# Kernel tuning notes

Measured on AMD Instinct MI355X. Metric: run time of the kernel, lower is better.

## Reference

```python
import jax, jax.numpy as jnp
import numpy as np

B, T = 512, 200
N_SKILLS, M, DK, DV, H = 1000, 50, 64, 64, 128


def setup_inputs() -> dict:
    key = jax.random.key(0)
    ks = jax.random.split(key, 12)
    inp = {
        'skill_seq': jax.random.randint(ks[0], (B, T), 0, N_SKILLS, dtype=jnp.int32),
        'correct_seq': jax.random.randint(ks[1], (B, T), 0, 2, dtype=jnp.int32),
        'mask': jnp.ones((B, T), dtype=jnp.float32),
        'skill_embed': jax.random.normal(ks[2], (N_SKILLS, DK), dtype=jnp.float32),
        'key_memory': jax.random.normal(ks[3], (M, DK), dtype=jnp.float32) * 0.1,
        'value_init': jnp.zeros((M, DV), dtype=jnp.float32),
        'interaction_embed': jax.random.normal(ks[4], (2 * N_SKILLS, DV), dtype=jnp.float32),
        'erase_W': jax.random.normal(ks[5], (DV, DV), dtype=jnp.float32) * 0.05,
        'erase_b': jnp.zeros((DV,), dtype=jnp.float32),
        'add_W': jax.random.normal(ks[6], (DV, DV), dtype=jnp.float32) * 0.05,
        'add_b': jnp.zeros((DV,), dtype=jnp.float32),
        'fc1_W': jax.random.normal(ks[7], (DK + DV, H), dtype=jnp.float32) * 0.05,
        'fc1_b': jnp.zeros((H,), dtype=jnp.float32),
        'fc2_W': jax.random.normal(ks[8], (H, 1), dtype=jnp.float32) * 0.05,
        'fc2_b': jnp.zeros((1,), dtype=jnp.float32),
    }
    return inp


def reference(skill_seq, correct_seq, mask, skill_embed, key_memory, value_init,
              interaction_embed, erase_W, erase_b, add_W, add_b,
              fc1_W, fc1_b, fc2_W, fc2_b):
    n_skills = skill_embed.shape[0]
    b = skill_seq.shape[0]
    # Time-invariant-per-step quantities are precomputed vectorized over (B,T):
    q = skill_embed[skill_seq]                                   # (B,T,dk)
    w = jax.nn.softmax(jnp.einsum('btk,mk->btm', q, key_memory), axis=-1)  # (B,T,M)
    v = interaction_embed[skill_seq + correct_seq * n_skills]    # (B,T,dv)
    e = jax.nn.sigmoid(v @ erase_W + erase_b)                    # (B,T,dv)
    a = jnp.tanh(v @ add_W + add_b)                              # (B,T,dv)

    def step(mem, inputs):
        # mem: (B,M,dv); read BEFORE write, matching the torch loop
        w_t, e_t, a_t = inputs                                   # (B,M),(B,dv),(B,dv)
        read = jnp.einsum('bm,bmv->bv', w_t, mem)                # (B,dv)
        we = w_t[:, :, None]                                     # (B,M,1)
        mem = mem * (1.0 - we * e_t[:, None, :]) + we * a_t[:, None, :]
        return mem, read

    mem0 = jnp.broadcast_to(value_init, (b,) + value_init.shape)
    _, reads = jax.lax.scan(step, mem0,
                            (jnp.swapaxes(w, 0, 1), jnp.swapaxes(e, 0, 1), jnp.swapaxes(a, 0, 1)))
    reads = jnp.swapaxes(reads, 0, 1)                            # (B,T,dv)

    x = jnp.concatenate([q, reads], axis=-1)                     # (B,T,dk+dv)
    h = jax.nn.relu(x @ fc1_W + fc1_b)
    logit = (h @ fc2_W + fc2_b)[..., 0]
    p = jax.nn.sigmoid(logit)
    return p * mask, correct_seq.astype(jnp.float32) * mask
```

## Files before the change

### kernel.cpp

```cpp
#include <hip/hip_runtime.h>
#include <hip/hip_bf16.h>

#define B_  512
#define T_  200
#define NS  1000
#define M_  50
#define DK  64
#define DV  64
#define H_  128
#define NPOS (B_ * T_)

typedef __hip_bfloat16 bf16;
typedef unsigned short ushort_t;
typedef __bf16 bf16x8 __attribute__((ext_vector_type(8)));
typedef float  f32x4  __attribute__((ext_vector_type(4)));

__device__ __forceinline__ float ldf(const void* p, int i, int isbf) {
    return isbf ? __bfloat162float(((const bf16*)p)[i]) : ((const float*)p)[i];
}
__device__ __forceinline__ int sniff(const void* mask) {
    return (*(const unsigned*)mask == 0x3F800000u) ? 0 : 1;
}
__device__ __forceinline__ float rl(float x, int l) {
    return __int_as_float(__builtin_amdgcn_readlane(__float_as_int(x), l));
}
__device__ __forceinline__ ushort_t f2bf(float v) {
    bf16 h = __float2bfloat16(v);
    return *(ushort_t*)&h;
}

__global__ __launch_bounds__(256) void dk20_tabs(
    const void* __restrict__ mask,
    const void* __restrict__ skill_embed, const void* __restrict__ key_memory,
    const void* __restrict__ inter,
    const void* __restrict__ eW, const void* __restrict__ eb,
    const void* __restrict__ aW, const void* __restrict__ ab,
    const void* __restrict__ fc1W, const void* __restrict__ fc1b,
    float* __restrict__ w_tab, unsigned* __restrict__ ea_tab,
    float* __restrict__ hq_tab, ushort_t* __restrict__ W2f) {
    int isbf = sniff(mask);
    int lane = threadIdx.x & 63;
    int gwid = (blockIdx.x << 2) | (threadIdx.x >> 6);

    if (gwid < NS) {
        int s = gwid;
        float q = ldf(skill_embed, s * DK + lane, isbf);
        float acc = 0.f;
        if (lane < M_) {
            #pragma unroll 16
            for (int k = 0; k < DK; ++k)
                acc = fmaf(rl(q, k), ldf(key_memory, lane * DK + k, isbf), acc);
        }
        float val = (lane < M_) ? acc : -1e30f;
        float mx = val;
        #pragma unroll
        for (int off = 1; off < 64; off <<= 1) mx = fmaxf(mx, __shfl_xor(mx, off, 64));
        float ex = (lane < M_) ? __expf(val - mx) : 0.f;
        float sm = ex;
        #pragma unroll
        for (int off = 1; off < 64; off <<= 1) sm += __shfl_xor(sm, off, 64);
        w_tab[s * 64 + lane] = (lane < M_) ? ex / sm : 0.f;
    } else if (gwid < 3 * NS) {
        int r = gwid - NS;
        float vv = ldf(inter, r * DV + lane, isbf);
        float eacc = ldf(eb, lane, isbf);
        float aacc = ldf(ab, lane, isbf);
        #pragma unroll 16
        for (int u = 0; u < DV; ++u) {
            float vu = rl(vv, u);
            eacc = fmaf(vu, ldf(eW, u * DV + lane, isbf), eacc);
            aacc = fmaf(vu, ldf(aW, u * DV + lane, isbf), aacc);
        }
        float ev = 1.f / (1.f + __expf(-eacc));
        float av = tanhf(aacc);
        ea_tab[r * 64 + lane] = ((unsigned)f2bf(av) << 16) | (unsigned)f2bf(ev);
    } else if (gwid < 4 * NS) {
        int s = gwid - 3 * NS;
        float q = ldf(skill_embed, s * DK + lane, isbf);
        float acc0 = ldf(fc1b, lane, isbf);
        float acc1 = ldf(fc1b, 64 + lane, isbf);
        #pragma unroll 16
        for (int k = 0; k < DK; ++k) {
            float qk = rl(q, k);
            acc0 = fmaf(qk, ldf(fc1W, k * H_ + lane, isbf), acc0);
            acc1 = fmaf(qk, ldf(fc1W, k * H_ + 64 + lane, isbf), acc1);
        }
        hq_tab[s * H_ + lane]      = acc0;
        hq_tab[s * H_ + 64 + lane] = acc1;
    } else if (gwid < 4 * NS + 16) {
        int f = gwid - 4 * NS;
        int tile = f >> 1, kk = f & 1;
        int n = tile * 16 + (lane & 15);
        #pragma unroll
        for (int j = 0; j < 8; ++j) {
            int v = kk * 32 + (lane >> 4) * 8 + j;
            W2f[(f * 64 + lane) * 8 + j] = f2bf(ldf(fc1W, (DK + v) * H_ + n, isbf));
        }
    }
}

#define SCAN_STEP(EA, WARR, TP) { \
    float e0 = __uint_as_float((EA) << 16); \
    float a0 = __uint_as_float((EA) & 0xFFFF0000u); \
    float acc0 = 0.f, acc1 = 0.f, acc2 = 0.f, acc3 = 0.f; \
    _Pragma("unroll") \
    for (int i = 0; i < 2; ++i) { \
        float4 w = WARR[i]; \
        acc0 = fmaf(w.x, mem[i].x, acc0); \
        acc1 = fmaf(w.y, mem[i].y, acc1); \
        acc2 = fmaf(w.z, mem[i].z, acc2); \
        acc3 = fmaf(w.w, mem[i].w, acc3); \
        mem[i].x = fmaf(-w.x, fmaf(e0, mem[i].x, -a0), mem[i].x); \
        mem[i].y = fmaf(-w.y, fmaf(e0, mem[i].y, -a0), mem[i].y); \
        mem[i].z = fmaf(-w.z, fmaf(e0, mem[i].z, -a0), mem[i].z); \
        mem[i].w = fmaf(-w.w, fmaf(e0, mem[i].w, -a0), mem[i].w); \
    } \
    red[buf][k][TP][lane] = (acc0 + acc1) + (acc2 + acc3); }

#define REFILL(EA, WARR) { \
    EA = ea_tab[(s2 + c2 * NS) * 64 + lane]; \
    WARR[0] = w4[s2 * 16 + 2 * k]; \
    WARR[1] = w4[s2 * 16 + 2 * k + 1]; }

#define ADV(TF) { s2 = s3; c2 = c3; int tf_ = (TF) < T_ ? (TF) : T_ - 1; \
    s3 = ss[base + tf_]; c3 = cs[base + tf_]; }

#define SUMSTORE(PB, CC) { \
    float s_ = red[PB][0][k][lane] + red[PB][1][k][lane] \
             + red[PB][2][k][lane] + red[PB][3][k][lane] \
             + red[PB][4][k][lane] + red[PB][5][k][lane] \
             + red[PB][6][k][lane] + red[PB][7][k][lane]; \
    read_bf[(size_t)(base + (CC) * 8 + k) * 64 + lane] = f2bf(s_); }

__global__ __launch_bounds__(512, 4) void dk20_scan(
    const int*  __restrict__ ss, const int* __restrict__ cs,
    const void* __restrict__ mask, const void* __restrict__ value_init,
    const float* __restrict__ w_tab, const unsigned* __restrict__ ea_tab,
    ushort_t* __restrict__ read_bf) {

    __shared__ float red[2][8][8][64];

    int isbf = sniff(mask);
    int lane = threadIdx.x & 63;
    int k    = threadIdx.x >> 6;
    int b    = blockIdx.x;
    const int base = b * T_;
    const int row0 = 8 * k;
    const float4* w4 = (const float4*)w_tab;

    float4 mem[2];
    #pragma unroll
    for (int i = 0; i < 2; ++i) {
        int r = row0 + 4 * i;
        mem[i].x = (r + 0 < M_) ? ldf(value_init, (r + 0) * DV + lane, isbf) : 0.f;
        mem[i].y = (r + 1 < M_) ? ldf(value_init, (r + 1) * DV + lane, isbf) : 0.f;
        mem[i].z = (r + 2 < M_) ? ldf(value_init, (r + 2) * DV + lane, isbf) : 0.f;
        mem[i].w = (r + 3 < M_) ? ldf(value_init, (r + 3) * DV + lane, isbf) : 0.f;
    }

    int s2 = ss[base + 2], c2 = cs[base + 2];
    int s3 = ss[base + 3], c3 = cs[base + 3];

    float4 wa[2], wb[2];
    unsigned eaA, eaB;
    {
        int sA = ss[base], cA = cs[base];
        eaA = ea_tab[(sA + cA * NS) * 64 + lane];
        wa[0] = w4[sA * 16 + 2 * k]; wa[1] = w4[sA * 16 + 2 * k + 1];
        int sB = ss[base + 1], cB = cs[base + 1];
        eaB = ea_tab[(sB + cB * NS) * 64 + lane];
        wb[0] = w4[sB * 16 + 2 * k]; wb[1] = w4[sB * 16 + 2 * k + 1];
    }

    for (int c = 0; c < 25; ++c) {
        int buf = c & 1;
        #pragma unroll
        for (int tp = 0; tp < 8; tp += 2) {
            int t = c * 8 + tp;
            SCAN_STEP(eaA, wa, tp)
            REFILL(eaA, wa)
            ADV(t + 4)
            SCAN_STEP(eaB, wb, tp + 1)
            REFILL(eaB, wb)
            ADV(t + 5)
        }
        if (c > 0) SUMSTORE((c - 1) & 1, c - 1)
        __syncthreads();
    }
    SUMSTORE(0, 24)
}

#define FOR8(X) X(0) X(1) X(2) X(3) X(4) X(5) X(6) X(7)
#define DECL_C(t)  f32x4 c##t = {0.f, 0.f, 0.f, 0.f};
#define LOADB(t) bf16x8 b##t##_0 = B8[(2 * (t)) * 64 + lane], \
                        b##t##_1 = B8[(2 * (t) + 1) * 64 + lane];
#define MFMA2(t) \
    c##t = __builtin_amdgcn_mfma_f32_16x16x32_bf16(a0, b##t##_0, c##t, 0, 0, 0); \
    c##t = __builtin_amdgcn_mfma_f32_16x16x32_bf16(a1, b##t##_1, c##t, 0, 0, 0);
#define EPI(t) { \
    float h; \
    h = c##t.x + hq_tab[s0r * H_ + t * 16 + col]; x0 = fmaf(fmaxf(h, 0.f), f2w##t, x0); \
    h = c##t.y + hq_tab[s1r * H_ + t * 16 + col]; x1 = fmaf(fmaxf(h, 0.f), f2w##t, x1); \
    h = c##t.z + hq_tab[s2r * H_ + t * 16 + col]; x2 = fmaf(fmaxf(h, 0.f), f2w##t, x2); \
    h = c##t.w + hq_tab[s3r * H_ + t * 16 + col]; x3 = fmaf(fmaxf(h, 0.f), f2w##t, x3); }

__global__ __launch_bounds__(64)
__attribute__((amdgpu_waves_per_eu(3))) void dk20_fc(
    const int*  __restrict__ skill_seq, const int* __restrict__ correct_seq,
    const void* __restrict__ mask,
    const void* __restrict__ fc2W, const void* __restrict__ fc2b,
    const float* __restrict__ hq_tab, const ushort_t* __restrict__ W2f,
    const ushort_t* __restrict__ read_bf,
    float* __restrict__ out0, float* __restrict__ out1) {

    int isbf = sniff(mask);
    int lane = threadIdx.x;
    int col  = lane & 15, quad = lane >> 4;

    const bf16x8* B8 = (const bf16x8*)W2f;
    FOR8(LOADB)

    float f2w0 = ldf(fc2W,   0 + col, isbf), f2w1 = ldf(fc2W,  16 + col, isbf);
    float f2w2 = ldf(fc2W,  32 + col, isbf), f2w3 = ldf(fc2W,  48 + col, isbf);
    float f2w4 = ldf(fc2W,  64 + col, isbf), f2w5 = ldf(fc2W,  80 + col, isbf);
    float f2w6 = ldf(fc2W,  96 + col, isbf), f2w7 = ldf(fc2W, 112 + col, isbf);
    float f2b  = ldf(fc2b, 0, isbf);

    for (int pg = blockIdx.x; pg < NPOS / 16; pg += gridDim.x) {
        int p0 = pg * 16;
        const bf16x8* A8 = (const bf16x8*)(read_bf + (size_t)p0 * 64);
        bf16x8 a0 = A8[col * 8 + quad];
        bf16x8 a1 = A8[col * 8 + 4 + quad];

        int s0r = skill_seq[p0 + quad * 4 + 0];
        int s1r = skill_seq[p0 + quad * 4 + 1];
        int s2r = skill_seq[p0 + quad * 4 + 2];
        int s3r = skill_seq[p0 + quad * 4 + 3];

        FOR8(DECL_C)
        FOR8(MFMA2)

        float x0 = 0.f, x1 = 0.f, x2 = 0.f, x3 = 0.f;
        FOR8(EPI)

        #pragma unroll
        for (int off = 1; off < 16; off <<= 1) {
            x0 += __shfl_xor(x0, off, 64);
            x1 += __shfl_xor(x1, off, 64);
            x2 += __shfl_xor(x2, off, 64);
            x3 += __shfl_xor(x3, off, 64);
        }

        float mk0 = ldf(mask, p0 + quad * 4 + 0, isbf);
        float mk1 = ldf(mask, p0 + quad * 4 + 1, isbf);
        float mk2 = ldf(mask, p0 + quad * 4 + 2, isbf);
        float mk3 = ldf(mask, p0 + quad * 4 + 3, isbf);
        if (col == 0) {
            out0[p0 + quad * 4 + 0] = mk0 / (1.f + __expf(-(x0 + f2b)));
            out0[p0 + quad * 4 + 1] = mk1 / (1.f + __expf(-(x1 + f2b)));
            out0[p0 + quad * 4 + 2] = mk2 / (1.f + __expf(-(x2 + f2b)));
            out0[p0 + quad * 4 + 3] = mk3 / (1.f + __expf(-(x3 + f2b)));
        }
        if (col == 1) {
            out1[p0 + quad * 4 + 0] = (float)correct_seq[p0 + quad * 4 + 0] * mk0;
            out1[p0 + quad * 4 + 1] = (float)correct_seq[p0 + quad * 4 + 1] * mk1;
            out1[p0 + quad * 4 + 2] = (float)correct_seq[p0 + quad * 4 + 2] * mk2;
            out1[p0 + quad * 4 + 3] = (float)correct_seq[p0 + quad * 4 + 3] * mk3;
        }
    }
}

extern "C" void kernel_launch(void* const* d_in, const int* in_sizes, int n_in,
                              void* d_out, int out_size, void* d_ws, size_t ws_size,
                              hipStream_t stream) {
    const int*  skill_seq   = (const int*)d_in[0];
    const int*  correct_seq = (const int*)d_in[1];
    const void* mask        = d_in[2];
    const void* skill_embed = d_in[3];
    const void* key_memory  = d_in[4];
    const void* value_init  = d_in[5];
    const void* inter       = d_in[6];
    const void* erase_W     = d_in[7];
    const void* erase_b     = d_in[8];
    const void* add_W       = d_in[9];
    const void* add_b       = d_in[10];
    const void* fc1_W       = d_in[11];
    const void* fc1_b       = d_in[12];
    const void* fc2_W       = d_in[13];
    const void* fc2_b       = d_in[14];
    float* out = (float*)d_out;

    float*    ws      = (float*)d_ws + 16;
    float*    w_tab   = ws;
    unsigned* ea_tab  = (unsigned*)(ws + 64000);
    float*    hq_tab  = ws + 192000;
    ushort_t* W2f     = (ushort_t*)(ws + 320000);
    ushort_t* read_bf = (ushort_t*)(ws + 336400);

    dk20_tabs<<<1004, 256, 0, stream>>>(mask, skill_embed, key_memory, inter,
                                        erase_W, erase_b, add_W, add_b,
                                        fc1_W, fc1_b,
                                        w_tab, ea_tab, hq_tab, W2f);

    dk20_scan<<<B_, 512, 0, stream>>>(skill_seq, correct_seq, mask, value_init,
                                      w_tab, ea_tab, read_bf);

    dk20_fc<<<3200, 64, 0, stream>>>(skill_seq, correct_seq, mask,
                                     fc2_W, fc2_b, hq_tab, W2f, read_bf,
                                     out, out + (size_t)NPOS);
}
```

Before: 180.6 us.

## Split scan memory rows across independent waves and fold partial-read reduction into FC MFMA

The scan kernel no longer uses one 512-thread block per batch row with a shared-memory reduction and a barrier after every 8 steps. It now runs four independent single-wave blocks per batch row, each owning 13 memory slots. The softmax weight table is repacked so each wave reads its 13 weights as three float4 loads plus one scalar. Each wave writes its partial read vector straight to global memory, and the FC kernel sums the four partials by treating them as a K=256 MFMA reduction that reuses the same fc1 weight fragments. This removes barriers and shared-memory traffic from the serial scan and raises block-level parallelism, at the cost of four times more read_bf traffic and workspace, plus extra MFMA work in the FC kernel.

```diff
diff --git a/kernel.cpp b/kernel.cpp
--- a/kernel.cpp
+++ b/kernel.cpp
@@ -29,7 +29,7 @@
     return *(ushort_t*)&h;
 }
 
-__global__ __launch_bounds__(256) void dk20_tabs(
+__global__ __launch_bounds__(256) void dk21_tabs(
     const void* __restrict__ mask,
     const void* __restrict__ skill_embed, const void* __restrict__ key_memory,
     const void* __restrict__ inter,
@@ -44,22 +44,25 @@
 
     if (gwid < NS) {
         int s = gwid;
+        int kq = lane >> 4, r = lane & 15;
+        int row = 13 * kq + r;
+        int valid = (r < 13) && (row < M_);
         float q = ldf(skill_embed, s * DK + lane, isbf);
         float acc = 0.f;
-        if (lane < M_) {
+        if (valid) {
             #pragma unroll 16
             for (int k = 0; k < DK; ++k)
-                acc = fmaf(rl(q, k), ldf(key_memory, lane * DK + k, isbf), acc);
-        }
-        float val = (lane < M_) ? acc : -1e30f;
+                acc = fmaf(rl(q, k), ldf(key_memory, row * DK + k, isbf), acc);
+        }
+        float val = valid ? acc : -1e30f;
         float mx = val;
         #pragma unroll
         for (int off = 1; off < 64; off <<= 1) mx = fmaxf(mx, __shfl_xor(mx, off, 64));
-        float ex = (lane < M_) ? __expf(val - mx) : 0.f;
+        float ex = valid ? __expf(val - mx) : 0.f;
         float sm = ex;
         #pragma unroll
         for (int off = 1; off < 64; off <<= 1) sm += __shfl_xor(sm, off, 64);
-        w_tab[s * 64 + lane] = (lane < M_) ? ex / sm : 0.f;
+        w_tab[s * 64 + lane] = valid ? ex / sm : 0.f;
     } else if (gwid < 3 * NS) {
         int r = gwid - NS;
         float vv = ldf(inter, r * DV + lane, isbf);
@@ -99,13 +102,14 @@
     }
 }
 
-#define SCAN_STEP(EA, WARR, TP) { \
-    float e0 = __uint_as_float((EA) << 16); \
-    float a0 = __uint_as_float((EA) & 0xFFFF0000u); \
+#define SC_STEP(D, TP) { \
+    unsigned ea = eas[D]; \
+    float e0 = __uint_as_float(ea << 16); \
+    float a0 = __uint_as_float(ea & 0xFFFF0000u); \
     float acc0 = 0.f, acc1 = 0.f, acc2 = 0.f, acc3 = 0.f; \
     _Pragma("unroll") \
-    for (int i = 0; i < 2; ++i) { \
-        float4 w = WARR[i]; \
+    for (int i = 0; i < 3; ++i) { \
+        float4 w = wst[D][i]; \
         acc0 = fmaf(w.x, mem[i].x, acc0); \
         acc1 = fmaf(w.y, mem[i].y, acc1); \
         acc2 = fmaf(w.z, mem[i].z, acc2); \
@@ -115,88 +119,82 @@
         mem[i].z = fmaf(-w.z, fmaf(e0, mem[i].z, -a0), mem[i].z); \
         mem[i].w = fmaf(-w.w, fmaf(e0, mem[i].w, -a0), mem[i].w); \
     } \
-    red[buf][k][TP][lane] = (acc0 + acc1) + (acc2 + acc3); }
-
-#define REFILL(EA, WARR) { \
-    EA = ea_tab[(s2 + c2 * NS) * 64 + lane]; \
-    WARR[0] = w4[s2 * 16 + 2 * k]; \
-    WARR[1] = w4[s2 * 16 + 2 * k + 1]; }
-
-#define ADV(TF) { s2 = s3; c2 = c3; int tf_ = (TF) < T_ ? (TF) : T_ - 1; \
-    s3 = ss[base + tf_]; c3 = cs[base + tf_]; }
-
-#define SUMSTORE(PB, CC) { \
-    float s_ = red[PB][0][k][lane] + red[PB][1][k][lane] \
-             + red[PB][2][k][lane] + red[PB][3][k][lane] \
-             + red[PB][4][k][lane] + red[PB][5][k][lane] \
-             + red[PB][6][k][lane] + red[PB][7][k][lane]; \
-    read_bf[(size_t)(base + (CC) * 8 + k) * 64 + lane] = f2bf(s_); }
-
-__global__ __launch_bounds__(512, 4) void dk20_scan(
+    float wS = w3[D]; \
+    acc0 = fmaf(wS, memS, acc0); \
+    memS = fmaf(-wS, fmaf(e0, memS, -a0), memS); \
+    *(ushort_t*)((char*)outp + (TP) * 512) = f2bf((acc0 + acc1) + (acc2 + acc3)); \
+    eas[D]    = ea_tab[(sA + cA * NS) * 64 + lane]; \
+    wst[D][0] = w4[sA * 16 + 4 * k + 0]; \
+    wst[D][1] = w4[sA * 16 + 4 * k + 1]; \
+    wst[D][2] = w4[sA * 16 + 4 * k + 2]; \
+    w3[D]     = w_tab[sA * 64 + 16 * k + 12]; \
+    sA = sB; cA = cB; \
+    { int tf_ = tbase + (TP) + 6; tf_ = tf_ < T_ ? tf_ : T_ - 1; \
+      sB = ss[base + tf_]; cB = cs[base + tf_]; } }
+
+__global__ __launch_bounds__(64, 2) void dk21_scan(
     const int*  __restrict__ ss, const int* __restrict__ cs,
     const void* __restrict__ mask, const void* __restrict__ value_init,
     const float* __restrict__ w_tab, const unsigned* __restrict__ ea_tab,
     ushort_t* __restrict__ read_bf) {
 
-    __shared__ float red[2][8][8][64];
-
     int isbf = sniff(mask);
-    int lane = threadIdx.x & 63;
-    int k    = threadIdx.x >> 6;
-    int b    = blockIdx.x;
+    int lane = threadIdx.x;
+    int bk   = blockIdx.x;
+    int b    = bk >> 2, k = bk & 3;
     const int base = b * T_;
-    const int row0 = 8 * k;
     const float4* w4 = (const float4*)w_tab;
 
-    float4 mem[2];
+    float4 mem[3]; float memS;
     #pragma unroll
-    for (int i = 0; i < 2; ++i) {
-        int r = row0 + 4 * i;
+    for (int i = 0; i < 3; ++i) {
+        int r = 13 * k + 4 * i;
         mem[i].x = (r + 0 < M_) ? ldf(value_init, (r + 0) * DV + lane, isbf) : 0.f;
         mem[i].y = (r + 1 < M_) ? ldf(value_init, (r + 1) * DV + lane, isbf) : 0.f;
         mem[i].z = (r + 2 < M_) ? ldf(value_init, (r + 2) * DV + lane, isbf) : 0.f;
         mem[i].w = (r + 3 < M_) ? ldf(value_init, (r + 3) * DV + lane, isbf) : 0.f;
     }
-
-    int s2 = ss[base + 2], c2 = cs[base + 2];
-    int s3 = ss[base + 3], c3 = cs[base + 3];
-
-    float4 wa[2], wb[2];
-    unsigned eaA, eaB;
-    {
-        int sA = ss[base], cA = cs[base];
-        eaA = ea_tab[(sA + cA * NS) * 64 + lane];
-        wa[0] = w4[sA * 16 + 2 * k]; wa[1] = w4[sA * 16 + 2 * k + 1];
-        int sB = ss[base + 1], cB = cs[base + 1];
-        eaB = ea_tab[(sB + cB * NS) * 64 + lane];
-        wb[0] = w4[sB * 16 + 2 * k]; wb[1] = w4[sB * 16 + 2 * k + 1];
-    }
-
-    for (int c = 0; c < 25; ++c) {
-        int buf = c & 1;
-        #pragma unroll
-        for (int tp = 0; tp < 8; tp += 2) {
-            int t = c * 8 + tp;
-            SCAN_STEP(eaA, wa, tp)
-            REFILL(eaA, wa)
-            ADV(t + 4)
-            SCAN_STEP(eaB, wb, tp + 1)
-            REFILL(eaB, wb)
-            ADV(t + 5)
-        }
-        if (c > 0) SUMSTORE((c - 1) & 1, c - 1)
-        __syncthreads();
-    }
-    SUMSTORE(0, 24)
+    { int r = 13 * k + 12; memS = (r < M_) ? ldf(value_init, r * DV + lane, isbf) : 0.f; }
+
+    float4   wst[4][3];
+    float    w3[4];
+    unsigned eas[4];
+    #pragma unroll
+    for (int d = 0; d < 4; ++d) {
+        int s = ss[base + d], c = cs[base + d];
+        eas[d]    = ea_tab[(s + c * NS) * 64 + lane];
+        wst[d][0] = w4[s * 16 + 4 * k + 0];
+        wst[d][1] = w4[s * 16 + 4 * k + 1];
+        wst[d][2] = w4[s * 16 + 4 * k + 2];
+        w3[d]     = w_tab[s * 64 + 16 * k + 12];
+    }
+    int sA = ss[base + 4], cA = cs[base + 4];
+    int sB = ss[base + 5], cB = cs[base + 5];
+
+    ushort_t* outp = read_bf + ((size_t)base * 4 + k) * 64 + lane;
+
+    for (int cc = 0; cc < 25; ++cc) {
+        int tbase = cc * 8;
+        SC_STEP(0, 0) SC_STEP(1, 1) SC_STEP(2, 2) SC_STEP(3, 3)
+        SC_STEP(0, 4) SC_STEP(1, 5) SC_STEP(2, 6) SC_STEP(3, 7)
+        outp += 2048;
+    }
 }
 
 #define FOR8(X) X(0) X(1) X(2) X(3) X(4) X(5) X(6) X(7)
 #define DECL_C(t)  f32x4 c##t = {0.f, 0.f, 0.f, 0.f};
 #define LOADB(t) bf16x8 b##t##_0 = B8[(2 * (t)) * 64 + lane], \
                         b##t##_1 = B8[(2 * (t) + 1) * 64 + lane];
-#define MFMA2(t) \
-    c##t = __builtin_amdgcn_mfma_f32_16x16x32_bf16(a0, b##t##_0, c##t, 0, 0, 0); \
-    c##t = __builtin_amdgcn_mfma_f32_16x16x32_bf16(a1, b##t##_1, c##t, 0, 0, 0);
+#define FCKK(kk, p) { \
+    bf16x8 av = A8[col * 32 + (kk) * 4 + quad]; \
+    c0 = __builtin_amdgcn_mfma_f32_16x16x32_bf16(av, b0_##p, c0, 0, 0, 0); \
+    c1 = __builtin_amdgcn_mfma_f32_16x16x32_bf16(av, b1_##p, c1, 0, 0, 0); \
+    c2 = __builtin_amdgcn_mfma_f32_16x16x32_bf16(av, b2_##p, c2, 0, 0, 0); \
+    c3 = __builtin_amdgcn_mfma_f32_16x16x32_bf16(av, b3_##p, c3, 0, 0, 0); \
+    c4 = __builtin_amdgcn_mfma_f32_16x16x32_bf16(av, b4_##p, c4, 0, 0, 0); \
+    c5 = __builtin_amdgcn_mfma_f32_16x16x32_bf16(av, b5_##p, c5, 0, 0, 0); \
+    c6 = __builtin_amdgcn_mfma_f32_16x16x32_bf16(av, b6_##p, c6, 0, 0, 0); \
+    c7 = __builtin_amdgcn_mfma_f32_16x16x32_bf16(av, b7_##p, c7, 0, 0, 0); }
 #define EPI(t) { \
     float h; \
     h = c##t.x + hq_tab[s0r * H_ + t * 16 + col]; x0 = fmaf(fmaxf(h, 0.f), f2w##t, x0); \
@@ -205,7 +203,7 @@
     h = c##t.w + hq_tab[s3r * H_ + t * 16 + col]; x3 = fmaf(fmaxf(h, 0.f), f2w##t, x3); }
 
 __global__ __launch_bounds__(64)
-__attribute__((amdgpu_waves_per_eu(3))) void dk20_fc(
+__attribute__((amdgpu_waves_per_eu(3))) void dk21_fc(
     const int*  __restrict__ skill_seq, const int* __restrict__ correct_seq,
     const void* __restrict__ mask,
     const void* __restrict__ fc2W, const void* __restrict__ fc2b,
@@ -228,9 +226,7 @@
 
     for (int pg = blockIdx.x; pg < NPOS / 16; pg += gridDim.x) {
         int p0 = pg * 16;
-        const bf16x8* A8 = (const bf16x8*)(read_bf + (size_t)p0 * 64);
-        bf16x8 a0 = A8[col * 8 + quad];
-        bf16x8 a1 = A8[col * 8 + 4 + quad];
+        const bf16x8* A8 = (const bf16x8*)(read_bf + (size_t)p0 * 256);
 
         int s0r = skill_seq[p0 + quad * 4 + 0];
         int s1r = skill_seq[p0 + quad * 4 + 1];
@@ -238,7 +234,8 @@
         int s3r = skill_seq[p0 + quad * 4 + 3];
 
         FOR8(DECL_C)
-        FOR8(MFMA2)
+        FCKK(0, 0) FCKK(1, 1) FCKK(2, 0) FCKK(3, 1)
+        FCKK(4, 0) FCKK(5, 1) FCKK(6, 0) FCKK(7, 1)
 
         float x0 = 0.f, x1 = 0.f, x2 = 0.f, x3 = 0.f;
         FOR8(EPI)
@@ -297,15 +294,15 @@
     ushort_t* W2f     = (ushort_t*)(ws + 320000);
     ushort_t* read_bf = (ushort_t*)(ws + 336400);
 
-    dk20_tabs<<<1004, 256, 0, stream>>>(mask, skill_embed, key_memory, inter,
+    dk21_tabs<<<1004, 256, 0, stream>>>(mask, skill_embed, key_memory, inter,
                                         erase_W, erase_b, add_W, add_b,
                                         fc1_W, fc1_b,
                                         w_tab, ea_tab, hq_tab, W2f);
 
-    dk20_scan<<<B_, 512, 0, stream>>>(skill_seq, correct_seq, mask, value_init,
-                                      w_tab, ea_tab, read_bf);
-
-    dk20_fc<<<3200, 64, 0, stream>>>(skill_seq, correct_seq, mask,
+    dk21_scan<<<B_ * 4, 64, 0, stream>>>(skill_seq, correct_seq, mask, value_init,
+                                         w_tab, ea_tab, read_bf);
+
+    dk21_fc<<<3200, 64, 0, stream>>>(skill_seq, correct_seq, mask,
                                      fc2_W, fc2_b, hq_tab, W2f, read_bf,
                                      out, out + (size_t)NPOS);
 }
```

Result: slower. 192.3 us (+6.5%).
